# Optimization experiments

Measured on AMD Instinct MI355X. Metric: run time of the kernel, lower is better.

Reference implementation:

```python
import jax, jax.numpy as jnp
import numpy as np

# Dimensions: batch B, time dims P,Q, grids N, hidden nhid
B, P, Q, N, NHID = 4, 6, 4, 512, 32
WD = 4 * NHID          # wd1 = wd2 = nhid*4 = 128
AD = 2 * WD            # ad = 2*nhid*4 = 256
ALPHA = 0.2            # LeakyReLU negative slope


def setup_inputs() -> dict:
    key = jax.random.key(0)
    k1, k2, k3, k4 = jax.random.split(key, 4)
    demand = jax.random.uniform(k1, (B, P, Q, N, N), dtype=jnp.float32)
    st_feat = jax.random.normal(k2, (B, P, Q, N, WD), dtype=jnp.float32)
    # xavier_uniform with gain=1.414
    lim_W = 1.414 * np.sqrt(6.0 / (WD + WD))
    W = jax.random.uniform(k3, (WD, WD), minval=-lim_W, maxval=lim_W, dtype=jnp.float32)
    lim_a = 1.414 * np.sqrt(6.0 / (AD + 1))
    a = jax.random.uniform(k4, (AD, 1), minval=-lim_a, maxval=lim_a, dtype=jnp.float32)
    return {"demand": demand, "st_feat": st_feat, "W": W, "a": a}


def reference(demand, st_feat, W, a):
    # h = st_feat @ W : [B,P,Q,N,WD]
    h = st_feat @ W
    # GAT algebraic split: a^T [h_i || h_j] = a1.h_i + a2.h_j
    # (same math as torch repeat/cat/matmul, without the O(N^2*AD) intermediate)
    a1 = a[:WD, 0]
    a2 = a[WD:, 0]
    s1 = h @ a1  # [B,P,Q,N] -- score contribution from node i (repeated rows)
    s2 = h @ a2  # [B,P,Q,N] -- score contribution from node j (tiled rows)
    e = jax.nn.leaky_relu(s1[..., :, None] + s2[..., None, :], negative_slope=ALPHA)
    attention = jax.nn.softmax(e, axis=-1)  # softmax over j (dim=4)
    # dropout omitted: eval-mode deterministic reference
    od_matrix = jax.nn.leaky_relu(demand * attention, negative_slope=ALPHA)
    return od_matrix
```

## Files before the change

### kernel.cpp

```cpp
#include <hip/hip_runtime.h>

#define NB 4
#define NP 6
#define NQ 4
#define NN 512
#define NWD 128
#define NROWS (NB * NP * NQ * NN)
#define ALPHA 0.2f

__device__ __forceinline__ float lrelu(float x) {
    return x > 0.f ? x : ALPHA * x;
}

__global__ __launch_bounds__(256) void s_fused_kernel(const float* __restrict__ st,
                                                      const float* __restrict__ W,
                                                      const float* __restrict__ a,
                                                      float* __restrict__ s1,
                                                      float* __restrict__ s2) {
    __shared__ float wa1[NWD];
    __shared__ float wa2[NWD];

    const int t = threadIdx.x;
    const int wid = t >> 6;
    const int lane = t & 63;

    {
        const int k = t & (NWD - 1);
        const float* av = a + (t >> 7) * NWD;
        const float* wr = W + (long)k * NWD;
        float s = 0.f;
        #pragma unroll
        for (int d = 0; d < NWD; d += 4) {
            const float4 wv  = *reinterpret_cast<const float4*>(wr + d);
            const float4 avv = *reinterpret_cast<const float4*>(av + d);
            s += wv.x * avv.x + wv.y * avv.y + wv.z * avv.z + wv.w * avv.w;
        }
        if (t < NWD) wa1[k] = s; else wa2[k] = s;
    }
    __syncthreads();

    const int l5 = lane & 31;
    const float4 w1v = *reinterpret_cast<const float4*>(&wa1[l5 * 4]);
    const float4 w2v = *reinterpret_cast<const float4*>(&wa2[l5 * 4]);
    const long blockbase = (long)blockIdx.x * 64;

    #pragma unroll
    for (int i = 0; i < 8; ++i) {
        const long rowpair = blockbase + (long)wid * 16 + i * 2;
        const float4 f = *reinterpret_cast<const float4*>(st + rowpair * NWD + lane * 4);
        float p1 = f.x * w1v.x + f.y * w1v.y + f.z * w1v.z + f.w * w1v.w;
        float p2 = f.x * w2v.x + f.y * w2v.y + f.z * w2v.z + f.w * w2v.w;
        #pragma unroll
        for (int off = 16; off > 0; off >>= 1) {
            p1 += __shfl_xor(p1, off);
            p2 += __shfl_xor(p2, off);
        }
        if (l5 == 0) {
            const long g = rowpair + (lane >> 5);
            s1[g] = p1;
            s2[g] = p2;
        }
    }
}

__global__ __launch_bounds__(256) void main_kernel(const float* __restrict__ demand,
                                                   const float* __restrict__ s1,
                                                   const float* __restrict__ s2,
                                                   float* __restrict__ out) {
    int wid = threadIdx.x >> 6;
    int lane = threadIdx.x & 63;
    long g = (long)blockIdx.x * 4 + wid;
    long slice = g >> 9;
    float s1i = s1[g];
    const float* s2s = s2 + slice * NN;

    const int c0 = lane * 4;
    const int c1 = 256 + lane * 4;
    const float4 sa = *reinterpret_cast<const float4*>(s2s + c0);
    const float4 sb = *reinterpret_cast<const float4*>(s2s + c1);

    float e[8];
    e[0] = lrelu(s1i + sa.x); e[1] = lrelu(s1i + sa.y);
    e[2] = lrelu(s1i + sa.z); e[3] = lrelu(s1i + sa.w);
    e[4] = lrelu(s1i + sb.x); e[5] = lrelu(s1i + sb.y);
    e[6] = lrelu(s1i + sb.z); e[7] = lrelu(s1i + sb.w);

    float m = e[0];
    #pragma unroll
    for (int k = 1; k < 8; ++k) m = fmaxf(m, e[k]);
    #pragma unroll
    for (int off = 32; off > 0; off >>= 1) m = fmaxf(m, __shfl_xor(m, off));

    float p[8];
    float sum = 0.f;
    #pragma unroll
    for (int k = 0; k < 8; ++k) { p[k] = __expf(e[k] - m); sum += p[k]; }
    #pragma unroll
    for (int off = 32; off > 0; off >>= 1) sum += __shfl_xor(sum, off);
    const float inv = 1.f / sum;

    const float* drow = demand + g * NN;
    const float4 d0 = *reinterpret_cast<const float4*>(drow + c0);
    const float4 d1 = *reinterpret_cast<const float4*>(drow + c1);

    float4 o0, o1;
    o0.x = lrelu(d0.x * p[0] * inv); o0.y = lrelu(d0.y * p[1] * inv);
    o0.z = lrelu(d0.z * p[2] * inv); o0.w = lrelu(d0.w * p[3] * inv);
    o1.x = lrelu(d1.x * p[4] * inv); o1.y = lrelu(d1.y * p[5] * inv);
    o1.z = lrelu(d1.z * p[6] * inv); o1.w = lrelu(d1.w * p[7] * inv);

    float* orow = out + g * NN;
    *reinterpret_cast<float4*>(orow + c0) = o0;
    *reinterpret_cast<float4*>(orow + c1) = o1;
}

extern "C" void kernel_launch(void* const* d_in, const int* in_sizes, int n_in,
                              void* d_out, int out_size, void* d_ws, size_t ws_size,
                              hipStream_t stream) {
    const float* demand  = (const float*)d_in[0];
    const float* st_feat = (const float*)d_in[1];
    const float* W       = (const float*)d_in[2];
    const float* a       = (const float*)d_in[3];
    float* out = (float*)d_out;

    float* s1 = (float*)d_ws;
    float* s2 = s1 + NROWS;

    s_fused_kernel<<<NROWS / 64, 256, 0, stream>>>(st_feat, W, a, s1, s2);
    main_kernel<<<NROWS / 4, 256, 0, stream>>>(demand, s1, s2, out);
}
```

Baseline: 54.07 us.

## Fuse score computation into softmax kernel with per-slice shared memory scores

Merges the two launches into one kernel where each block recomputes W·a and the s1/s2 scores for its whole slice into shared memory, then processes 64 rows of the attention/output. It also replaces the per-row max reduction with an analytic max via lrelu monotonicity. This removes the workspace round trip and a launch, but each slice's features are re-read by 8 blocks and each block does a serial prologue before streaming demand.

```diff
diff --git a/kernel.cpp b/kernel.cpp
--- a/kernel.cpp
+++ b/kernel.cpp
@@ -1,117 +1,131 @@
 #include <hip/hip_runtime.h>
 
-#define NB 4
-#define NP 6
-#define NQ 4
 #define NN 512
 #define NWD 128
-#define NROWS (NB * NP * NQ * NN)
+#define NSLICES 96
+#define NROWS (NSLICES * NN)
+#define BLOCKS_PER_SLICE 8
+#define ROWS_PER_BLOCK (NN / BLOCKS_PER_SLICE)
+#define NBLOCKS (NSLICES * BLOCKS_PER_SLICE)
 #define ALPHA 0.2f
 
 __device__ __forceinline__ float lrelu(float x) {
     return x > 0.f ? x : ALPHA * x;
 }
 
-__global__ __launch_bounds__(256) void s_fused_kernel(const float* __restrict__ st,
-                                                      const float* __restrict__ W,
-                                                      const float* __restrict__ a,
-                                                      float* __restrict__ s1,
-                                                      float* __restrict__ s2) {
+__global__ __launch_bounds__(256) void fused_kernel(const float* __restrict__ demand,
+                                                    const float* __restrict__ st,
+                                                    const float* __restrict__ W,
+                                                    const float* __restrict__ a,
+                                                    float* __restrict__ out) {
     __shared__ float wa1[NWD];
     __shared__ float wa2[NWD];
+    __shared__ float s1All[NN];
+    __shared__ float s2All[NN];
+    __shared__ float wmax[4];
 
     const int t = threadIdx.x;
     const int wid = t >> 6;
     const int lane = t & 63;
+    const int l5 = lane & 31;
+    const int half = lane >> 5;
+
+    const int p = blockIdx.x;
+    const int b = (p & 7) * (NBLOCKS / 8) + (p >> 3);
+    const int slice = b >> 3;
+    const int rowblk = (b & 7) * ROWS_PER_BLOCK;
+
+    const float* stS = st + (long)slice * NN * NWD;
 
     {
-        const int k = t & (NWD - 1);
-        const float* av = a + (t >> 7) * NWD;
-        const float* wr = W + (long)k * NWD;
-        float s = 0.f;
+        const float4 a1v = *reinterpret_cast<const float4*>(a + l5 * 4);
+        const float4 a2v = *reinterpret_cast<const float4*>(a + NWD + l5 * 4);
         #pragma unroll
-        for (int d = 0; d < NWD; d += 4) {
-            const float4 wv  = *reinterpret_cast<const float4*>(wr + d);
-            const float4 avv = *reinterpret_cast<const float4*>(av + d);
-            s += wv.x * avv.x + wv.y * avv.y + wv.z * avv.z + wv.w * avv.w;
+        for (int i = 0; i < 16; ++i) {
+            const int k = wid * 32 + i * 2;
+            const float4 wv = *reinterpret_cast<const float4*>(W + (long)k * NWD + lane * 4);
+            float p1 = wv.x * a1v.x + wv.y * a1v.y + wv.z * a1v.z + wv.w * a1v.w;
+            float p2 = wv.x * a2v.x + wv.y * a2v.y + wv.z * a2v.z + wv.w * a2v.w;
+            #pragma unroll
+            for (int off = 16; off > 0; off >>= 1) {
+                p1 += __shfl_xor(p1, off);
+                p2 += __shfl_xor(p2, off);
+            }
+            if (l5 == 0) { wa1[k + half] = p1; wa2[k + half] = p2; }
         }
-        if (t < NWD) wa1[k] = s; else wa2[k] = s;
     }
     __syncthreads();
 
-    const int l5 = lane & 31;
-    const float4 w1v = *reinterpret_cast<const float4*>(&wa1[l5 * 4]);
-    const float4 w2v = *reinterpret_cast<const float4*>(&wa2[l5 * 4]);
-    const long blockbase = (long)blockIdx.x * 64;
-
-    #pragma unroll
-    for (int i = 0; i < 8; ++i) {
-        const long rowpair = blockbase + (long)wid * 16 + i * 2;
-        const float4 f = *reinterpret_cast<const float4*>(st + rowpair * NWD + lane * 4);
-        float p1 = f.x * w1v.x + f.y * w1v.y + f.z * w1v.z + f.w * w1v.w;
-        float p2 = f.x * w2v.x + f.y * w2v.y + f.z * w2v.z + f.w * w2v.w;
-        #pragma unroll
-        for (int off = 16; off > 0; off >>= 1) {
-            p1 += __shfl_xor(p1, off);
-            p2 += __shfl_xor(p2, off);
-        }
-        if (l5 == 0) {
-            const long g = rowpair + (lane >> 5);
-            s1[g] = p1;
-            s2[g] = p2;
+    {
+        const float4 w1v = *reinterpret_cast<const float4*>(&wa1[l5 * 4]);
+        const float4 w2v = *reinterpret_cast<const float4*>(&wa2[l5 * 4]);
+        #pragma unroll 4
+        for (int i = 0; i < 64; ++i) {
+            const int r = wid * 128 + i * 2;
+            const float4 f = *reinterpret_cast<const float4*>(stS + (long)r * NWD + lane * 4);
+            float p1 = f.x * w1v.x + f.y * w1v.y + f.z * w1v.z + f.w * w1v.w;
+            float p2 = f.x * w2v.x + f.y * w2v.y + f.z * w2v.z + f.w * w2v.w;
+            #pragma unroll
+            for (int off = 16; off > 0; off >>= 1) {
+                p1 += __shfl_xor(p1, off);
+                p2 += __shfl_xor(p2, off);
+            }
+            if (l5 == 0) { s1All[r + half] = p1; s2All[r + half] = p2; }
         }
     }
-}
+    __syncthreads();
 
-__global__ __launch_bounds__(256) void main_kernel(const float* __restrict__ demand,
-                                                   const float* __restrict__ s1,
-                                                   const float* __restrict__ s2,
-                                                   float* __restrict__ out) {
-    int wid = threadIdx.x >> 6;
-    int lane = threadIdx.x & 63;
-    long g = (long)blockIdx.x * 4 + wid;
-    long slice = g >> 9;
-    float s1i = s1[g];
-    const float* s2s = s2 + slice * NN;
+    {
+        float ml = fmaxf(s2All[t], s2All[t + 256]);
+        #pragma unroll
+        for (int off = 32; off > 0; off >>= 1) ml = fmaxf(ml, __shfl_xor(ml, off));
+        if (lane == 0) wmax[wid] = ml;
+    }
+    __syncthreads();
+    const float M = fmaxf(fmaxf(wmax[0], wmax[1]), fmaxf(wmax[2], wmax[3]));
 
     const int c0 = lane * 4;
     const int c1 = 256 + lane * 4;
-    const float4 sa = *reinterpret_cast<const float4*>(s2s + c0);
-    const float4 sb = *reinterpret_cast<const float4*>(s2s + c1);
+    const float4 sa = *reinterpret_cast<const float4*>(&s2All[c0]);
+    const float4 sb = *reinterpret_cast<const float4*>(&s2All[c1]);
 
-    float e[8];
-    e[0] = lrelu(s1i + sa.x); e[1] = lrelu(s1i + sa.y);
-    e[2] = lrelu(s1i + sa.z); e[3] = lrelu(s1i + sa.w);
-    e[4] = lrelu(s1i + sb.x); e[5] = lrelu(s1i + sb.y);
-    e[6] = lrelu(s1i + sb.z); e[7] = lrelu(s1i + sb.w);
+    for (int i = 0; i < 16; ++i) {
+        const int row = rowblk + wid * 16 + i;
+        const long g = (long)slice * NN + row;
+        const float s1i = s1All[row];
+        const float m = lrelu(s1i + M);
 
-    float m = e[0];
-    #pragma unroll
-    for (int k = 1; k < 8; ++k) m = fmaxf(m, e[k]);
-    #pragma unroll
-    for (int off = 32; off > 0; off >>= 1) m = fmaxf(m, __shfl_xor(m, off));
+        float pv[8];
+        pv[0] = __expf(lrelu(s1i + sa.x) - m);
+        pv[1] = __expf(lrelu(s1i + sa.y) - m);
+        pv[2] = __expf(lrelu(s1i + sa.z) - m);
+        pv[3] = __expf(lrelu(s1i + sa.w) - m);
+        pv[4] = __expf(lrelu(s1i + sb.x) - m);
+        pv[5] = __expf(lrelu(s1i + sb.y) - m);
+        pv[6] = __expf(lrelu(s1i + sb.z) - m);
+        pv[7] = __expf(lrelu(s1i + sb.w) - m);
 
-    float p[8];
-    float sum = 0.f;
-    #pragma unroll
-    for (int k = 0; k < 8; ++k) { p[k] = __expf(e[k] - m); sum += p[k]; }
-    #pragma unroll
-    for (int off = 32; off > 0; off >>= 1) sum += __shfl_xor(sum, off);
-    const float inv = 1.f / sum;
+        float sum = 0.f;
+        #pragma unroll
+        for (int k = 0; k < 8; ++k) sum += pv[k];
+        #pragma unroll
+        for (int off = 32; off > 0; off >>= 1) sum += __shfl_xor(sum, off);
+        const float inv = 1.f / sum;
 
-    const float* drow = demand + g * NN;
-    const float4 d0 = *reinterpret_cast<const float4*>(drow + c0);
-    const float4 d1 = *reinterpret_cast<const float4*>(drow + c1);
+        const float* drow = demand + g * NN;
+        const float4 d0 = *reinterpret_cast<const float4*>(drow + c0);
+        const float4 d1 = *reinterpret_cast<const float4*>(drow + c1);
 
-    float4 o0, o1;
-    o0.x = lrelu(d0.x * p[0] * inv); o0.y = lrelu(d0.y * p[1] * inv);
-    o0.z = lrelu(d0.z * p[2] * inv); o0.w = lrelu(d0.w * p[3] * inv);
-    o1.x = lrelu(d1.x * p[4] * inv); o1.y = lrelu(d1.y * p[5] * inv);
-    o1.z = lrelu(d1.z * p[6] * inv); o1.w = lrelu(d1.w * p[7] * inv);
+        float4 o0, o1;
+        o0.x = lrelu(d0.x * pv[0] * inv); o0.y = lrelu(d0.y * pv[1] * inv);
+        o0.z = lrelu(d0.z * pv[2] * inv); o0.w = lrelu(d0.w * pv[3] * inv);
+        o1.x = lrelu(d1.x * pv[4] * inv); o1.y = lrelu(d1.y * pv[5] * inv);
+        o1.z = lrelu(d1.z * pv[6] * inv); o1.w = lrelu(d1.w * pv[7] * inv);
 
-    float* orow = out + g * NN;
-    *reinterpret_cast<float4*>(orow + c0) = o0;
-    *reinterpret_cast<float4*>(orow + c1) = o1;
+        float* orow = out + g * NN;
+        *reinterpret_cast<float4*>(orow + c0) = o0;
+        *reinterpret_cast<float4*>(orow + c1) = o1;
+    }
 }
 
 extern "C" void kernel_launch(void* const* d_in, const int* in_sizes, int n_in,
@@ -123,9 +137,5 @@
     const float* a       = (const float*)d_in[3];
     float* out = (float*)d_out;
 
-    float* s1 = (float*)d_ws;
-    float* s2 = s1 + NROWS;
-
-    s_fused_kernel<<<NROWS / 64, 256, 0, stream>>>(st_feat, W, a, s1, s2);
-    main_kernel<<<NROWS / 4, 256, 0, stream>>>(demand, s1, s2, out);
+    fused_kernel<<<NBLOCKS, 256, 0, stream>>>(demand, st_feat, W, a, out);
 }
```

Measured after the change: 72.97 us. +35.0%, slower.
